# Kernel optimization log

Measured on AMD Instinct MI355X. Metric: run time of the kernel, lower is better.

## Reference

```python
import jax, jax.numpy as jnp
import numpy as np

NUM_LAYERS = 10
HIDDEN = 5
INPUT = 5
SEQ = 457
OUT = 457


def _lstm_layer(x_tbi, W_ih, W_hh, b):
    # x_tbi: [T, B, in]; W_ih: [4H, in]; W_hh: [4H, H]; b: [4H] (b_ih + b_hh)
    B = x_tbi.shape[1]
    h0 = jnp.zeros((B, HIDDEN), x_tbi.dtype)
    c0 = jnp.zeros((B, HIDDEN), x_tbi.dtype)
    # precompute input projections for all timesteps: [T, B, 4H]
    xW = jnp.einsum('tbi,gi->tbg', x_tbi, W_ih) + b

    def step(carry, xw_t):
        h, c = carry
        gates = xw_t + h @ W_hh.T  # [B, 4H]
        i, f, g, o = jnp.split(gates, 4, axis=-1)  # PyTorch gate order i,f,g,o
        i = jax.nn.sigmoid(i)
        f = jax.nn.sigmoid(f)
        g = jnp.tanh(g)
        o = jax.nn.sigmoid(o)
        c = f * c + i * g
        h = o * jnp.tanh(c)
        return (h, c), h

    (_, _), hs = jax.lax.scan(step, (h0, c0), xW)
    return hs  # [T, B, H]


def setup_inputs() -> dict:
    key = jax.random.key(0)
    ks = jax.random.split(key, 8)
    B = 4096
    x = jax.random.normal(ks[0], (B, SEQ, INPUT), dtype=jnp.float32)
    attn = jnp.ones((B, SEQ), dtype=jnp.int64)
    tok = jnp.zeros((B, SEQ), dtype=jnp.int64)
    s = 1.0 / np.sqrt(HIDDEN)
    # layer 0 input size == HIDDEN, so all layers stack uniformly
    W_ih = jax.random.uniform(ks[1], (NUM_LAYERS, 4 * HIDDEN, INPUT), jnp.float32, -s, s)
    W_hh = jax.random.uniform(ks[2], (NUM_LAYERS, 4 * HIDDEN, HIDDEN), jnp.float32, -s, s)
    b_ih = jax.random.uniform(ks[3], (NUM_LAYERS, 4 * HIDDEN), jnp.float32, -s, s)
    b_hh = jax.random.uniform(ks[4], (NUM_LAYERS, 4 * HIDDEN), jnp.float32, -s, s)
    sf = 1.0 / np.sqrt(HIDDEN * SEQ)
    fc_W = jax.random.uniform(ks[5], (OUT, HIDDEN * SEQ), jnp.float32, -sf, sf)
    fc_b = jax.random.uniform(ks[6], (OUT,), jnp.float32, -sf, sf)
    return {"a_input_ids": x, "a_attention_mask": attn, "a_token_type_ids": tok,
            "W_ih": W_ih, "W_hh": W_hh, "b_ih": b_ih, "b_hh": b_hh,
            "fc_W": fc_W, "fc_b": fc_b}


def reference(a_input_ids, a_attention_mask, a_token_type_ids, W_ih, W_hh, b_ih, b_hh, fc_W, fc_b):
    x = jnp.transpose(a_input_ids.astype(jnp.float32), (1, 0, 2))  # [T, B, 5]
    b = b_ih + b_hh
    for l in range(NUM_LAYERS):
        x = _lstm_layer(x, W_ih[l], W_hh[l], b[l])  # [T, B, H]
    out = jnp.transpose(x, (1, 0, 2))  # [B, T, H]
    flat = out.reshape(out.shape[0], -1)  # [B, T*H]
    # dropout is identity at inference
    return flat @ fc_W.T + fc_b  # [B, OUT]
```

## Files before the change

### kernel.cpp

```cpp
#include <hip/hip_runtime.h>

#define NUM_LAYERS 10
#define HIDDEN 5
#define SEQ 457
#define BATCH 4096
#define OUT_DIM 457
#define KD 2285
#define KPAD 2304
#define NKT 72
#define OPAD 512

typedef __attribute__((ext_vector_type(8))) short short8;
typedef __attribute__((ext_vector_type(4))) float f32x4;
typedef unsigned long long ull;
typedef unsigned short ushort;

__device__ __forceinline__ float frcp(float x){ return __builtin_amdgcn_rcpf(x); }
__device__ __forceinline__ float fexp2(float x){ return __builtin_amdgcn_exp2f(x); }
__device__ __forceinline__ ushort f2bf(float f){
    unsigned u = __float_as_uint(f);
    u = (u + 0x7FFFu + ((u>>16)&1u)) >> 16;
    return (ushort)u;
}
__device__ __forceinline__ float bf2f(ushort h){ return __uint_as_float(((unsigned)h) << 16); }
__device__ __forceinline__ unsigned cvtpk(float a, float b){
    unsigned r;
    asm("v_cvt_pk_bf16_f32 %0, %1, %2" : "=v"(r) : "v"(a), "v"(b));
    return r;
}
__device__ __forceinline__ void act4(const f32x4 d, float& i_, float& f_, float& g_, float& o_){
    i_ = frcp(1.f + fexp2(d[0]));
    f_ = frcp(1.f + fexp2(d[1]));
    g_ = 1.f - 2.f*frcp(1.f + fexp2(d[2]));
    o_ = frcp(1.f + fexp2(d[3]));
}
__device__ __forceinline__ float tanhc(float c){ return 1.f - 2.f*frcp(1.f + fexp2(2.8853900817779268f*c)); }

#define GB 16
#define NW 11
#define BUFS 6400

__global__ __launch_bounds__(64*NW) void lstm_kernel(
    const float* __restrict__ x,
    const float* __restrict__ W_ih,
    const float* __restrict__ W_hh,
    const float* __restrict__ b_ih,
    const float* __restrict__ b_hh,
    ushort* __restrict__ HbP)
{
    __shared__ ull CsQ[3200];
    ushort* Cs = (ushort*)CsQ;
    const int tid = threadIdx.x;
    const int lane = tid & 63;
    const int lS = __builtin_amdgcn_readfirstlane(tid >> 6);
    const int bg = blockIdx.x;
    const int hbBase = bg * (NKT*512);

    for (int i = tid; i < 3200; i += 64*NW) CsQ[i] = 0;
    __syncthreads();

    const int m  = lane & 15;
    const int kg = lane >> 4;

    short8 wf0{}, wf1{};
    f32x4 bias0{}, bias1{};
    float c0 = 0.f, c4 = 0.f;
    float xr0=0,xr1=0,xr2=0,xr3=0,xr4=0;
    const float* xb2 = nullptr;
    const int half = lane >> 4;
    const int gb = lane & 15;

    const char* rd0 = nullptr; const char* rd1 = nullptr;
    ushort* myP = nullptr; ushort* j4P = nullptr;
    char* gw = nullptr;

    if (lS < NUM_LAYERS) {
        const int l = lS;
        {
            const int j = m >> 2, g = m & 3;
            const float scg = (g == 2) ? 2.8853900817779268f : -1.4426950408889634f;
            const int row = l*20 + g*5 + j;
#pragma unroll
            for (int e = 0; e < 8; ++e) {
                const int k = kg*8 + e;
                ushort v = 0;
                if (k < 30) {
                    const int ki = (k < 10) ? k : (k < 20) ? k-10 : k-20;
                    const float w = scg * ((ki < 5) ? W_ih[row*5+ki] : W_hh[row*5+ki-5]);
                    const ushort hi = f2bf(w);
                    v = (k >= 20) ? f2bf(w - bf2f(hi)) : hi;
                }
                wf0[e] = (short)v;
            }
        }
        {
#pragma unroll
            for (int e = 0; e < 8; ++e) {
                ushort v = 0;
                if (m < 4) {
                    const int g = m;
                    const float scg = (g == 2) ? 2.8853900817779268f : -1.4426950408889634f;
                    const int row = l*20 + g*5 + 4;
                    const int k = kg*8 + e;
                    if (k < 30) {
                        const int ki = (k < 10) ? k : (k < 20) ? k-10 : k-20;
                        const float w = scg * ((ki < 5) ? W_ih[row*5+ki] : W_hh[row*5+ki-5]);
                        const ushort hi = f2bf(w);
                        v = (k >= 20) ? f2bf(w - bf2f(hi)) : hi;
                    }
                }
                wf1[e] = (short)v;
            }
        }
#pragma unroll
        for (int r = 0; r < 4; ++r) {
            const float scg = (r == 2) ? 2.8853900817779268f : -1.4426950408889634f;
            bias0[r] = scg * (b_ih[l*20 + r*5 + kg] + b_hh[l*20 + r*5 + kg]);
            bias1[r] = (kg == 0) ? scg * (b_ih[l*20 + r*5 + 4] + b_hh[l*20 + r*5 + 4]) : 0.f;
        }
        const int off0 = (kg==0) ? 0 : (kg==1) ? 16 : (kg==2) ? 32 : 8;
        const int off1 = (kg==0) ? 8 : (kg==1) ? 24 : (kg==2) ? 0 : 16;
        const int slotB = (l*16 + m) * 80;
        rd0 = (const char*)Cs + slotB + off0;
        rd1 = (const char*)Cs + slotB + off1;
        myP = Cs + (l*16 + m)*40 + kg;
        j4P = Cs + (l*16 + m)*40;
    } else {
        if (lane < 32) {
            xb2 = x + (size_t)(bg*GB + gb) * (SEQ*HIDDEN);
            gw = (char*)Cs + gb*80 + half*40;
        }
        ull* slab = (ull*)(HbP + hbBase + 71*512);
        slab[lane] = 0; slab[lane + 64] = 0;
    }
    __syncthreads();

    if (lS == NUM_LAYERS && lane < 32) {
        float v0 = xb2[half*5+0], v1 = xb2[half*5+1], v2 = xb2[half*5+2],
              v3 = xb2[half*5+3], v4 = xb2[half*5+4];
        unsigned p01 = cvtpk(v0,v1), p23 = cvtpk(v2,v3);
        ushort p4 = f2bf(v4);
        float l0 = v0 - __uint_as_float(p01<<16), l1 = v1 - __uint_as_float(p01 & 0xFFFF0000u);
        float l2 = v2 - __uint_as_float(p23<<16), l3 = v3 - __uint_as_float(p23 & 0xFFFF0000u);
        float l4 = v4 - bf2f(p4);
        unsigned q01 = cvtpk(l0,l1), q23 = cvtpk(l2,l3);
        *(unsigned*)(gw + 0)  = p01;
        *(unsigned*)(gw + 4)  = p23;
        *(ushort*)  (gw + 8)  = p4;
        *(unsigned*)(gw + 20) = q01;
        *(unsigned*)(gw + 24) = q23;
        *(ushort*)  (gw + 28) = f2bf(l4);
        xr0 = xb2[(2+half)*5+0]; xr1 = xb2[(2+half)*5+1]; xr2 = xb2[(2+half)*5+2];
        xr3 = xb2[(2+half)*5+3]; xr4 = xb2[(2+half)*5+4];
    }
    __syncthreads();

    int s = 0;
    auto cell = [&](int PP) {
        const int WP = 1 - PP;
        const int t0 = 2*(s - lS);
        const bool a0 = (t0 >= 0) & (t0 <= SEQ-1);
        const bool a1 = (t0 >= 0) & (t0 <  SEQ-1);
        union { short8 v; ull q[2]; } bf;
        bf.q[0] = *(const ull*)(rd0 + PP*12800);
        bf.q[1] = *(const ull*)(rd1 + PP*12800);
        f32x4 d0 = __builtin_amdgcn_mfma_f32_16x16x32_bf16(wf0, bf.v, bias0, 0,0,0);
        f32x4 d4 = __builtin_amdgcn_mfma_f32_16x16x32_bf16(wf1, bf.v, bias1, 0,0,0);
        float ig,fg,gg,og, i4,f4,g4,o4;
        act4(d0, ig,fg,gg,og);
        act4(d4, i4,f4,g4,o4);
        if (a0) {
            c0 = fg*c0 + ig*gg;
            const float h = og * tanhc(c0);
            c4 = f4*c4 + i4*g4;
            const float h4 = o4 * tanhc(c4);
            const unsigned ph = cvtpk(h, h4);
            const unsigned pl = cvtpk(h - __uint_as_float(ph<<16),
                                      h4 - __uint_as_float(ph & 0xFFFF0000u));
            myP[PP*BUFS + 25] = (ushort)ph;
            myP[PP*BUFS + 35] = (ushort)pl;
            if (kg == 0) { j4P[PP*BUFS + 29] = (ushort)(ph>>16); j4P[PP*BUFS + 39] = (ushort)(pl>>16); }
            if (lS < NUM_LAYERS-1) {
                myP[WP*BUFS + 640] = (ushort)ph;
                myP[WP*BUFS + 650] = (ushort)pl;
                if (kg == 0) { j4P[WP*BUFS + 644] = (ushort)(ph>>16); j4P[WP*BUFS + 654] = (ushort)(pl>>16); }
            } else {
                const int k = t0*5 + kg;
                HbP[hbBase + (k>>5)*512 + ((k>>3)&3)*128 + m*8 + (k&7)] = (ushort)ph;
                if (kg == 0) {
                    const int k4 = t0*5 + 4;
                    HbP[hbBase + (k4>>5)*512 + ((k4>>3)&3)*128 + m*8 + (k4&7)] = (ushort)(ph>>16);
                }
            }
        }
        bf.q[0] = *(const ull*)(rd0 + PP*12800 + 40);
        bf.q[1] = *(const ull*)(rd1 + PP*12800 + 40);
        d0 = __builtin_amdgcn_mfma_f32_16x16x32_bf16(wf0, bf.v, bias0, 0,0,0);
        d4 = __builtin_amdgcn_mfma_f32_16x16x32_bf16(wf1, bf.v, bias1, 0,0,0);
        act4(d0, ig,fg,gg,og);
        act4(d4, i4,f4,g4,o4);
        if (a1) {
            c0 = fg*c0 + ig*gg;
            const float h = og * tanhc(c0);
            c4 = f4*c4 + i4*g4;
            const float h4 = o4 * tanhc(c4);
            const unsigned ph = cvtpk(h, h4);
            const unsigned pl = cvtpk(h - __uint_as_float(ph<<16),
                                      h4 - __uint_as_float(ph & 0xFFFF0000u));
            myP[WP*BUFS + 5]  = (ushort)ph;
            myP[WP*BUFS + 15] = (ushort)pl;
            if (kg == 0) { j4P[WP*BUFS + 9] = (ushort)(ph>>16); j4P[WP*BUFS + 19] = (ushort)(pl>>16); }
            if (lS < NUM_LAYERS-1) {
                myP[WP*BUFS + 660] = (ushort)ph;
                myP[WP*BUFS + 670] = (ushort)pl;
                if (kg == 0) { j4P[WP*BUFS + 664] = (ushort)(ph>>16); j4P[WP*BUFS + 674] = (ushort)(pl>>16); }
            } else {
                const int k = (t0+1)*5 + kg;
                HbP[hbBase + (k>>5)*512 + ((k>>3)&3)*128 + m*8 + (k&7)] = (ushort)ph;
                if (kg == 0) {
                    const int k4 = (t0+1)*5 + 4;
                    HbP[hbBase + (k4>>5)*512 + ((k4>>3)&3)*128 + m*8 + (k4&7)] = (ushort)(ph>>16);
                }
            }
        }
    };
    auto ghost = [&](int PP) {
        const int WP = 1 - PP;
        if (lane < 32) {
            const int tw = 2*s + 2 + half;
            if (tw < SEQ) {
                unsigned p01 = cvtpk(xr0,xr1), p23 = cvtpk(xr2,xr3);
                ushort p4 = f2bf(xr4);
                float l0 = xr0 - __uint_as_float(p01<<16), l1 = xr1 - __uint_as_float(p01 & 0xFFFF0000u);
                float l2 = xr2 - __uint_as_float(p23<<16), l3 = xr3 - __uint_as_float(p23 & 0xFFFF0000u);
                float l4 = xr4 - bf2f(p4);
                unsigned q01 = cvtpk(l0,l1), q23 = cvtpk(l2,l3);
                *(unsigned*)(gw + WP*12800 + 0)  = p01;
                *(unsigned*)(gw + WP*12800 + 4)  = p23;
                *(ushort*)  (gw + WP*12800 + 8)  = p4;
                *(unsigned*)(gw + WP*12800 + 20) = q01;
                *(unsigned*)(gw + WP*12800 + 24) = q23;
                *(ushort*)  (gw + WP*12800 + 28) = f2bf(l4);
            }
            int tn = 2*s + 4 + half; if (tn > SEQ-1) tn = SEQ-1;
            xr0 = xb2[tn*5+0]; xr1 = xb2[tn*5+1]; xr2 = xb2[tn*5+2];
            xr3 = xb2[tn*5+3]; xr4 = xb2[tn*5+4];
        }
    };

    for (int it = 0; it < 119; ++it) {
        if (lS < NUM_LAYERS) cell(0); else ghost(0);
        __syncthreads(); ++s;
        if (lS < NUM_LAYERS) cell(1); else ghost(1);
        __syncthreads(); ++s;
    }
}

__global__ __launch_bounds__(256) void convw_kernel(
    const float* __restrict__ fcW,
    ushort* __restrict__ WhiP,
    ushort* __restrict__ WloP)
{
    const int tidg = blockIdx.x * 256 + threadIdx.x;
    if (tidg >= 32*NKT*64) return;
    const int L  = tidg & 63;
    const int kk = (tidg >> 6) % NKT;
    const int og = tidg / (64*NKT);
    const int o = og*16 + (L & 15);
    const int kb = kk*32 + ((L >> 4) << 3);
    short8 hi8{}, lo8{};
#pragma unroll
    for (int e = 0; e < 8; ++e) {
        const int k = kb + e;
        float v = 0.f;
        if (o < OUT_DIM && k < KD) v = fcW[(size_t)o*KD + k];
        const ushort hi = f2bf(v);
        hi8[e] = (short)hi;
        lo8[e] = (short)f2bf(v - bf2f(hi));
    }
    *(short8*)&WhiP[(size_t)tidg*8] = hi8;
    *(short8*)&WloP[(size_t)tidg*8] = lo8;
}

__global__ __launch_bounds__(256) void fc_kernel(
    const ushort* __restrict__ HbP,
    const ushort* __restrict__ WhiP,
    const ushort* __restrict__ WloP,
    const float* __restrict__ fcb,
    float* __restrict__ out)
{
    const int lane = threadIdx.x & 63;
    const int w = threadIdx.x >> 6;
    const int bgi = blockIdx.x*4 + w;
    const int ogB = blockIdx.y*4;
    const ushort* Ap  = HbP  + (size_t)bgi*(NKT*512) + lane*8;
    const ushort* Wh0 = WhiP + (size_t)(ogB+0)*(NKT*512) + lane*8;
    const ushort* Wh1 = WhiP + (size_t)(ogB+1)*(NKT*512) + lane*8;
    const ushort* Wh2 = WhiP + (size_t)(ogB+2)*(NKT*512) + lane*8;
    const ushort* Wh3 = WhiP + (size_t)(ogB+3)*(NKT*512) + lane*8;
    const ushort* Wl0 = WloP + (size_t)(ogB+0)*(NKT*512) + lane*8;
    const ushort* Wl1 = WloP + (size_t)(ogB+1)*(NKT*512) + lane*8;
    const ushort* Wl2 = WloP + (size_t)(ogB+2)*(NKT*512) + lane*8;
    const ushort* Wl3 = WloP + (size_t)(ogB+3)*(NKT*512) + lane*8;

    f32x4 acc0{}, acc1{}, acc2{}, acc3{};

    short8 a_c   = *(const short8*)(Ap);
    short8 wh0_c = *(const short8*)(Wh0);
    short8 wh1_c = *(const short8*)(Wh1);
    short8 wh2_c = *(const short8*)(Wh2);
    short8 wh3_c = *(const short8*)(Wh3);
    short8 wl0_c = *(const short8*)(Wl0);
    short8 wl1_c = *(const short8*)(Wl1);
    short8 wl2_c = *(const short8*)(Wl2);
    short8 wl3_c = *(const short8*)(Wl3);

    for (int kk = 0; kk < NKT; ++kk) {
        const int kb = (kk+1 < NKT) ? (kk+1)*512 : kk*512;
        const short8 a_n   = *(const short8*)(Ap  + kb);
        const short8 wh0_n = *(const short8*)(Wh0 + kb);
        const short8 wh1_n = *(const short8*)(Wh1 + kb);
        const short8 wh2_n = *(const short8*)(Wh2 + kb);
        const short8 wh3_n = *(const short8*)(Wh3 + kb);
        const short8 wl0_n = *(const short8*)(Wl0 + kb);
        const short8 wl1_n = *(const short8*)(Wl1 + kb);
        const short8 wl2_n = *(const short8*)(Wl2 + kb);
        const short8 wl3_n = *(const short8*)(Wl3 + kb);

        acc0 = __builtin_amdgcn_mfma_f32_16x16x32_bf16(a_c, wh0_c, acc0, 0,0,0);
        acc1 = __builtin_amdgcn_mfma_f32_16x16x32_bf16(a_c, wh1_c, acc1, 0,0,0);
        acc2 = __builtin_amdgcn_mfma_f32_16x16x32_bf16(a_c, wh2_c, acc2, 0,0,0);
        acc3 = __builtin_amdgcn_mfma_f32_16x16x32_bf16(a_c, wh3_c, acc3, 0,0,0);
        acc0 = __builtin_amdgcn_mfma_f32_16x16x32_bf16(a_c, wl0_c, acc0, 0,0,0);
        acc1 = __builtin_amdgcn_mfma_f32_16x16x32_bf16(a_c, wl1_c, acc1, 0,0,0);
        acc2 = __builtin_amdgcn_mfma_f32_16x16x32_bf16(a_c, wl2_c, acc2, 0,0,0);
        acc3 = __builtin_amdgcn_mfma_f32_16x16x32_bf16(a_c, wl3_c, acc3, 0,0,0);

        a_c = a_n;
        wh0_c = wh0_n; wh1_c = wh1_n; wh2_c = wh2_n; wh3_c = wh3_n;
        wl0_c = wl0_n; wl1_c = wl1_n; wl2_c = wl2_n; wl3_c = wl3_n;
    }

    const int ocol = lane & 15;
    const int br0 = (lane >> 4) * 4;
    const int b0 = bgi * 16;
#pragma unroll
    for (int nb = 0; nb < 4; ++nb) {
        const int o = (ogB + nb)*16 + ocol;
        if (o < OUT_DIM) {
            const float bias = fcb[o];
            const f32x4 acc = (nb==0) ? acc0 : (nb==1) ? acc1 : (nb==2) ? acc2 : acc3;
#pragma unroll
            for (int r = 0; r < 4; ++r) {
                out[(size_t)(b0 + br0 + r)*OUT_DIM + o] = acc[r] + bias;
            }
        }
    }
}

extern "C" void kernel_launch(void* const* d_in, const int* in_sizes, int n_in,
                              void* d_out, int out_size, void* d_ws, size_t ws_size,
                              hipStream_t stream) {
    const float* x    = (const float*)d_in[0];
    const float* W_ih = (const float*)d_in[3];
    const float* W_hh = (const float*)d_in[4];
    const float* b_ih = (const float*)d_in[5];
    const float* b_hh = (const float*)d_in[6];
    const float* fcW  = (const float*)d_in[7];
    const float* fcb  = (const float*)d_in[8];
    float* out = (float*)d_out;

    ushort* HbP  = (ushort*)d_ws;
    ushort* WhiP = (ushort*)((char*)d_ws + (size_t)256*NKT*512*2);
    ushort* WloP = (ushort*)((char*)d_ws + (size_t)256*NKT*512*2 + (size_t)32*NKT*512*2);

    lstm_kernel<<<dim3(BATCH/GB), dim3(64*NW), 0, stream>>>(
        x, W_ih, W_hh, b_ih, b_hh, HbP);

    convw_kernel<<<dim3((32*NKT*64 + 255)/256), dim3(256), 0, stream>>>(fcW, WhiP, WloP);

    fc_kernel<<<dim3(64, 8), dim3(256), 0, stream>>>(HbP, WhiP, WloP, fcb, out);
}
```

Before: 488.9 us.

## Process four timesteps per barrier interval in wavefront LSTM pipeline

The layer-wavefront LSTM now advances each layer by four timesteps between block barriers instead of two. The shared-memory staging is reorganised into per-row slots holding four sub-steps, with the ghost wave staging four input timesteps at a time. This roughly halves the number of __syncthreads across the whole recurrence, and so the pipeline skew, at the cost of larger LDS buffers. Separately, the FC kernel moves to 512-thread blocks, giving 8 wave batch groups per block instead of 4.

```diff
diff --git a/kernel.cpp b/kernel.cpp
--- a/kernel.cpp
+++ b/kernel.cpp
@@ -6,7 +6,6 @@
 #define BATCH 4096
 #define OUT_DIM 457
 #define KD 2285
-#define KPAD 2304
 #define NKT 72
 #define OPAD 512
 
@@ -28,6 +27,8 @@
     asm("v_cvt_pk_bf16_f32 %0, %1, %2" : "=v"(r) : "v"(a), "v"(b));
     return r;
 }
+__device__ __forceinline__ float lo16f(unsigned p){ return __uint_as_float(p << 16); }
+__device__ __forceinline__ float hi16f(unsigned p){ return __uint_as_float(p & 0xFFFF0000u); }
 __device__ __forceinline__ void act4(const f32x4 d, float& i_, float& f_, float& g_, float& o_){
     i_ = frcp(1.f + fexp2(d[0]));
     f_ = frcp(1.f + fexp2(d[1]));
@@ -38,7 +39,11 @@
 
 #define GB 16
 #define NW 11
-#define BUFS 6400
+#define SUB_SH 20
+#define SLOT_SH 92
+#define LBUF_SH (NUM_LAYERS*GB*SLOT_SH)
+#define LBUF_B  (LBUF_SH*2)
+#define NINT 124
 
 __global__ __launch_bounds__(64*NW) void lstm_kernel(
     const float* __restrict__ x,
@@ -48,15 +53,15 @@
     const float* __restrict__ b_hh,
     ushort* __restrict__ HbP)
 {
-    __shared__ ull CsQ[3200];
+    __shared__ ull CsQ[2*LBUF_SH/4];
     ushort* Cs = (ushort*)CsQ;
     const int tid = threadIdx.x;
     const int lane = tid & 63;
     const int lS = __builtin_amdgcn_readfirstlane(tid >> 6);
     const int bg = blockIdx.x;
-    const int hbBase = bg * (NKT*512);
-
-    for (int i = tid; i < 3200; i += 64*NW) CsQ[i] = 0;
+    const size_t hbBase = (size_t)bg * (NKT*512);
+
+    for (int i = tid; i < 2*LBUF_SH/4; i += 64*NW) CsQ[i] = 0;
     __syncthreads();
 
     const int m  = lane & 15;
@@ -67,12 +72,11 @@
     float c0 = 0.f, c4 = 0.f;
     float xr0=0,xr1=0,xr2=0,xr3=0,xr4=0;
     const float* xb2 = nullptr;
-    const int half = lane >> 4;
-    const int gb = lane & 15;
-
-    const char* rd0 = nullptr; const char* rd1 = nullptr;
-    ushort* myP = nullptr; ushort* j4P = nullptr;
-    char* gw = nullptr;
+    const int tt4 = lane >> 4;
+    const char* rdB = nullptr;
+    int off0 = 0, off1 = 0;
+    int slotSh = 0;
+    char* gw0 = nullptr;
 
     if (lS < NUM_LAYERS) {
         const int l = lS;
@@ -118,141 +122,94 @@
             bias0[r] = scg * (b_ih[l*20 + r*5 + kg] + b_hh[l*20 + r*5 + kg]);
             bias1[r] = (kg == 0) ? scg * (b_ih[l*20 + r*5 + 4] + b_hh[l*20 + r*5 + 4]) : 0.f;
         }
-        const int off0 = (kg==0) ? 0 : (kg==1) ? 16 : (kg==2) ? 32 : 8;
-        const int off1 = (kg==0) ? 8 : (kg==1) ? 24 : (kg==2) ? 0 : 16;
-        const int slotB = (l*16 + m) * 80;
-        rd0 = (const char*)Cs + slotB + off0;
-        rd1 = (const char*)Cs + slotB + off1;
-        myP = Cs + (l*16 + m)*40 + kg;
-        j4P = Cs + (l*16 + m)*40;
+        off0 = (kg==0) ? 0 : (kg==1) ? 16 : (kg==2) ? 32 : 8;
+        off1 = (kg==0) ? 8 : (kg==1) ? 24 : (kg==2) ? 0 : 16;
+        slotSh = (l*16 + m) * SLOT_SH;
+        rdB = (const char*)Cs + slotSh*2;
     } else {
-        if (lane < 32) {
-            xb2 = x + (size_t)(bg*GB + gb) * (SEQ*HIDDEN);
-            gw = (char*)Cs + gb*80 + half*40;
-        }
+        xb2 = x + (size_t)(bg*GB + m) * (SEQ*HIDDEN);
+        gw0 = (char*)Cs + (m*SLOT_SH + tt4*SUB_SH)*2;
         ull* slab = (ull*)(HbP + hbBase + 71*512);
         slab[lane] = 0; slab[lane + 64] = 0;
     }
     __syncthreads();
 
-    if (lS == NUM_LAYERS && lane < 32) {
-        float v0 = xb2[half*5+0], v1 = xb2[half*5+1], v2 = xb2[half*5+2],
-              v3 = xb2[half*5+3], v4 = xb2[half*5+4];
-        unsigned p01 = cvtpk(v0,v1), p23 = cvtpk(v2,v3);
-        ushort p4 = f2bf(v4);
-        float l0 = v0 - __uint_as_float(p01<<16), l1 = v1 - __uint_as_float(p01 & 0xFFFF0000u);
-        float l2 = v2 - __uint_as_float(p23<<16), l3 = v3 - __uint_as_float(p23 & 0xFFFF0000u);
-        float l4 = v4 - bf2f(p4);
-        unsigned q01 = cvtpk(l0,l1), q23 = cvtpk(l2,l3);
-        *(unsigned*)(gw + 0)  = p01;
-        *(unsigned*)(gw + 4)  = p23;
-        *(ushort*)  (gw + 8)  = p4;
-        *(unsigned*)(gw + 20) = q01;
-        *(unsigned*)(gw + 24) = q23;
-        *(ushort*)  (gw + 28) = f2bf(l4);
-        xr0 = xb2[(2+half)*5+0]; xr1 = xb2[(2+half)*5+1]; xr2 = xb2[(2+half)*5+2];
-        xr3 = xb2[(2+half)*5+3]; xr4 = xb2[(2+half)*5+4];
+    if (lS == NUM_LAYERS) {
+        const float v0=xb2[tt4*5+0], v1=xb2[tt4*5+1], v2=xb2[tt4*5+2],
+                    v3=xb2[tt4*5+3], v4=xb2[tt4*5+4];
+        const unsigned p01=cvtpk(v0,v1), p23=cvtpk(v2,v3);
+        const unsigned q01=cvtpk(v0-lo16f(p01), v1-hi16f(p01)),
+                       q23=cvtpk(v2-lo16f(p23), v3-hi16f(p23));
+        const ushort p4=f2bf(v4);
+        *(unsigned*)(gw0+0)=p01;  *(unsigned*)(gw0+4)=p23;  *(ushort*)(gw0+8)=p4;
+        *(unsigned*)(gw0+20)=q01; *(unsigned*)(gw0+24)=q23; *(ushort*)(gw0+28)=f2bf(v4-bf2f(p4));
+        xr0=xb2[(4+tt4)*5+0]; xr1=xb2[(4+tt4)*5+1]; xr2=xb2[(4+tt4)*5+2];
+        xr3=xb2[(4+tt4)*5+3]; xr4=xb2[(4+tt4)*5+4];
     }
     __syncthreads();
 
-    int s = 0;
-    auto cell = [&](int PP) {
-        const int WP = 1 - PP;
-        const int t0 = 2*(s - lS);
-        const bool a0 = (t0 >= 0) & (t0 <= SEQ-1);
-        const bool a1 = (t0 >= 0) & (t0 <  SEQ-1);
-        union { short8 v; ull q[2]; } bf;
-        bf.q[0] = *(const ull*)(rd0 + PP*12800);
-        bf.q[1] = *(const ull*)(rd1 + PP*12800);
-        f32x4 d0 = __builtin_amdgcn_mfma_f32_16x16x32_bf16(wf0, bf.v, bias0, 0,0,0);
-        f32x4 d4 = __builtin_amdgcn_mfma_f32_16x16x32_bf16(wf1, bf.v, bias1, 0,0,0);
-        float ig,fg,gg,og, i4,f4,g4,o4;
-        act4(d0, ig,fg,gg,og);
-        act4(d4, i4,f4,g4,o4);
-        if (a0) {
-            c0 = fg*c0 + ig*gg;
-            const float h = og * tanhc(c0);
-            c4 = f4*c4 + i4*g4;
-            const float h4 = o4 * tanhc(c4);
-            const unsigned ph = cvtpk(h, h4);
-            const unsigned pl = cvtpk(h - __uint_as_float(ph<<16),
-                                      h4 - __uint_as_float(ph & 0xFFFF0000u));
-            myP[PP*BUFS + 25] = (ushort)ph;
-            myP[PP*BUFS + 35] = (ushort)pl;
-            if (kg == 0) { j4P[PP*BUFS + 29] = (ushort)(ph>>16); j4P[PP*BUFS + 39] = (ushort)(pl>>16); }
-            if (lS < NUM_LAYERS-1) {
-                myP[WP*BUFS + 640] = (ushort)ph;
-                myP[WP*BUFS + 650] = (ushort)pl;
-                if (kg == 0) { j4P[WP*BUFS + 644] = (ushort)(ph>>16); j4P[WP*BUFS + 654] = (ushort)(pl>>16); }
-            } else {
-                const int k = t0*5 + kg;
-                HbP[hbBase + (k>>5)*512 + ((k>>3)&3)*128 + m*8 + (k&7)] = (ushort)ph;
-                if (kg == 0) {
-                    const int k4 = t0*5 + 4;
-                    HbP[hbBase + (k4>>5)*512 + ((k4>>3)&3)*128 + m*8 + (k4&7)] = (ushort)(ph>>16);
+    int cur = 0;
+    for (int s = 0; s < NINT; ++s) {
+        if (lS < NUM_LAYERS) {
+            const int t0 = 4*(s - lS);
+            const char* rbase = rdB + cur*LBUF_B;
+            ushort* curS = Cs + cur*LBUF_SH + slotSh;
+            ushort* nxtS = Cs + (cur^1)*LBUF_SH + slotSh;
+            ushort* nxtN = nxtS + 16*SLOT_SH;
+#pragma unroll
+            for (int tt = 0; tt < 4; ++tt) {
+                union { short8 v; ull q[2]; } bf;
+                bf.q[0] = *(const ull*)(rbase + tt*40 + off0);
+                bf.q[1] = *(const ull*)(rbase + tt*40 + off1);
+                f32x4 d0 = __builtin_amdgcn_mfma_f32_16x16x32_bf16(wf0, bf.v, bias0, 0,0,0);
+                f32x4 d4 = __builtin_amdgcn_mfma_f32_16x16x32_bf16(wf1, bf.v, bias1, 0,0,0);
+                float ig,fg,gg,og, i4,f4,g4,o4;
+                act4(d0, ig,fg,gg,og);
+                act4(d4, i4,f4,g4,o4);
+                const int t = t0 + tt;
+                if (t >= 0 && t < SEQ) {
+                    c0 = fg*c0 + ig*gg;
+                    const float h0 = og * tanhc(c0);
+                    c4 = f4*c4 + i4*g4;
+                    const float h4 = o4 * tanhc(c4);
+                    const unsigned ph = cvtpk(h0, h4);
+                    const unsigned pl = cvtpk(h0 - lo16f(ph), h4 - hi16f(ph));
+                    ushort* ownH = (tt < 3) ? (curS + (tt+1)*SUB_SH) : nxtS;
+                    ownH[5+kg]  = (ushort)ph;
+                    ownH[15+kg] = (ushort)pl;
+                    if (kg == 0) { ownH[9] = (ushort)(ph>>16); ownH[19] = (ushort)(pl>>16); }
+                    if (lS < NUM_LAYERS-1) {
+                        ushort* nin = nxtN + tt*SUB_SH;
+                        nin[kg]    = (ushort)ph;
+                        nin[10+kg] = (ushort)pl;
+                        if (kg == 0) { nin[4] = (ushort)(ph>>16); nin[14] = (ushort)(pl>>16); }
+                    } else {
+                        const int k = t*5 + kg;
+                        HbP[hbBase + (k>>5)*512 + ((k>>3)&3)*128 + m*8 + (k&7)] = (ushort)ph;
+                        if (kg == 0) {
+                            const int k4 = t*5 + 4;
+                            HbP[hbBase + (k4>>5)*512 + ((k4>>3)&3)*128 + m*8 + (k4&7)] = (ushort)(ph>>16);
+                        }
+                    }
                 }
             }
-        }
-        bf.q[0] = *(const ull*)(rd0 + PP*12800 + 40);
-        bf.q[1] = *(const ull*)(rd1 + PP*12800 + 40);
-        d0 = __builtin_amdgcn_mfma_f32_16x16x32_bf16(wf0, bf.v, bias0, 0,0,0);
-        d4 = __builtin_amdgcn_mfma_f32_16x16x32_bf16(wf1, bf.v, bias1, 0,0,0);
-        act4(d0, ig,fg,gg,og);
-        act4(d4, i4,f4,g4,o4);
-        if (a1) {
-            c0 = fg*c0 + ig*gg;
-            const float h = og * tanhc(c0);
-            c4 = f4*c4 + i4*g4;
-            const float h4 = o4 * tanhc(c4);
-            const unsigned ph = cvtpk(h, h4);
-            const unsigned pl = cvtpk(h - __uint_as_float(ph<<16),
-                                      h4 - __uint_as_float(ph & 0xFFFF0000u));
-            myP[WP*BUFS + 5]  = (ushort)ph;
-            myP[WP*BUFS + 15] = (ushort)pl;
-            if (kg == 0) { j4P[WP*BUFS + 9] = (ushort)(ph>>16); j4P[WP*BUFS + 19] = (ushort)(pl>>16); }
-            if (lS < NUM_LAYERS-1) {
-                myP[WP*BUFS + 660] = (ushort)ph;
-                myP[WP*BUFS + 670] = (ushort)pl;
-                if (kg == 0) { j4P[WP*BUFS + 664] = (ushort)(ph>>16); j4P[WP*BUFS + 674] = (ushort)(pl>>16); }
-            } else {
-                const int k = (t0+1)*5 + kg;
-                HbP[hbBase + (k>>5)*512 + ((k>>3)&3)*128 + m*8 + (k&7)] = (ushort)ph;
-                if (kg == 0) {
-                    const int k4 = (t0+1)*5 + 4;
-                    HbP[hbBase + (k4>>5)*512 + ((k4>>3)&3)*128 + m*8 + (k4&7)] = (ushort)(ph>>16);
-                }
-            }
-        }
-    };
-    auto ghost = [&](int PP) {
-        const int WP = 1 - PP;
-        if (lane < 32) {
-            const int tw = 2*s + 2 + half;
+        } else {
+            const int tw = 4*(s+1) + tt4;
+            char* gw = gw0 + (cur^1)*LBUF_B;
             if (tw < SEQ) {
-                unsigned p01 = cvtpk(xr0,xr1), p23 = cvtpk(xr2,xr3);
-                ushort p4 = f2bf(xr4);
-                float l0 = xr0 - __uint_as_float(p01<<16), l1 = xr1 - __uint_as_float(p01 & 0xFFFF0000u);
-                float l2 = xr2 - __uint_as_float(p23<<16), l3 = xr3 - __uint_as_float(p23 & 0xFFFF0000u);
-                float l4 = xr4 - bf2f(p4);
-                unsigned q01 = cvtpk(l0,l1), q23 = cvtpk(l2,l3);
-                *(unsigned*)(gw + WP*12800 + 0)  = p01;
-                *(unsigned*)(gw + WP*12800 + 4)  = p23;
-                *(ushort*)  (gw + WP*12800 + 8)  = p4;
-                *(unsigned*)(gw + WP*12800 + 20) = q01;
-                *(unsigned*)(gw + WP*12800 + 24) = q23;
-                *(ushort*)  (gw + WP*12800 + 28) = f2bf(l4);
-            }
-            int tn = 2*s + 4 + half; if (tn > SEQ-1) tn = SEQ-1;
-            xr0 = xb2[tn*5+0]; xr1 = xb2[tn*5+1]; xr2 = xb2[tn*5+2];
-            xr3 = xb2[tn*5+3]; xr4 = xb2[tn*5+4];
-        }
-    };
-
-    for (int it = 0; it < 119; ++it) {
-        if (lS < NUM_LAYERS) cell(0); else ghost(0);
-        __syncthreads(); ++s;
-        if (lS < NUM_LAYERS) cell(1); else ghost(1);
-        __syncthreads(); ++s;
+                const unsigned p01=cvtpk(xr0,xr1), p23=cvtpk(xr2,xr3);
+                const unsigned q01=cvtpk(xr0-lo16f(p01), xr1-hi16f(p01)),
+                               q23=cvtpk(xr2-lo16f(p23), xr3-hi16f(p23));
+                const ushort p4=f2bf(xr4);
+                *(unsigned*)(gw+0)=p01;  *(unsigned*)(gw+4)=p23;  *(ushort*)(gw+8)=p4;
+                *(unsigned*)(gw+20)=q01; *(unsigned*)(gw+24)=q23; *(ushort*)(gw+28)=f2bf(xr4-bf2f(p4));
+            }
+            int tn = 4*(s+2) + tt4; if (tn > SEQ-1) tn = SEQ-1;
+            xr0=xb2[tn*5+0]; xr1=xb2[tn*5+1]; xr2=xb2[tn*5+2];
+            xr3=xb2[tn*5+3]; xr4=xb2[tn*5+4];
+        }
+        __syncthreads();
+        cur ^= 1;
     }
 }
 
@@ -282,7 +239,7 @@
     *(short8*)&WloP[(size_t)tidg*8] = lo8;
 }
 
-__global__ __launch_bounds__(256) void fc_kernel(
+__global__ __launch_bounds__(512) void fc_kernel(
     const ushort* __restrict__ HbP,
     const ushort* __restrict__ WhiP,
     const ushort* __restrict__ WloP,
@@ -291,7 +248,7 @@
 {
     const int lane = threadIdx.x & 63;
     const int w = threadIdx.x >> 6;
-    const int bgi = blockIdx.x*4 + w;
+    const int bgi = blockIdx.x*8 + w;
     const int ogB = blockIdx.y*4;
     const ushort* Ap  = HbP  + (size_t)bgi*(NKT*512) + lane*8;
     const ushort* Wh0 = WhiP + (size_t)(ogB+0)*(NKT*512) + lane*8;
@@ -379,5 +336,5 @@
 
     convw_kernel<<<dim3((32*NKT*64 + 255)/256), dim3(256), 0, stream>>>(fcW, WhiP, WloP);
 
-    fc_kernel<<<dim3(64, 8), dim3(256), 0, stream>>>(HbP, WhiP, WloP, fcb, out);
-}
+    fc_kernel<<<dim3(32, 8), dim3(512), 0, stream>>>(HbP, WhiP, WloP, fcb, out);
+}
```

Result: no change. 494.2 us (+1.1%).
